# Kernel tuning notes

Hardware: AMD Instinct MI355X
Metric: run time of the kernel (lower is better)

Reference implementation:

```python
import jax, jax.numpy as jnp
import numpy as np

N_IN, D_IN, N_OUT, D_OUT = 1152, 8, 10, 16
ROUTINGS, NUM_BG = 3, 1
C, H, W = 1, 28, 28
BATCH = 128
DEC_IN = N_OUT * D_OUT  # 160, projection_type=None -> dec_feature_size = outcaps_size


def squash(x, axis=-1):
    norm = jnp.linalg.norm(x, axis=axis, keepdims=True)
    scale = norm ** 2 / (1.0 + norm ** 2) / (norm + 1e-8)
    return scale * x


def scale_coef(x, num_bg):
    # x: [B, n_out] or [B, n_out, n_in]; min/max normalize over dim 1,
    # excluding the last num_bg (background) capsules, then floor at 0.5.
    if num_bg > 0:
        xm = x[:, : x.shape[1] - num_bg]
    else:
        xm = x
    mn = jnp.min(xm, axis=1, keepdims=True)
    mx = jnp.max(xm, axis=1, keepdims=True)
    out = (xm - mn) / jnp.maximum(mx - mn, 1e-6)  # vrange (0,1)
    if num_bg > 0:
        out = jnp.concatenate([out, jnp.zeros_like(out[:, :num_bg])], axis=1)
    return jnp.maximum(out, 0.5)


def decode(capsflat, W1, b1, W2, b2, W3, b3):
    # fcn decoder (eval mode: dropout is identity): 160 -> 512 -> 1024 -> C*H*W
    h = jax.nn.relu(capsflat @ W1 + b1)
    h = jax.nn.relu(h @ W2 + b2)
    return jax.nn.sigmoid(h @ W3 + b3)


def setup_inputs() -> dict:
    key = jax.random.key(0)
    ks = jax.random.split(key, 9)
    return {
        'incaps': jax.random.normal(ks[0], (BATCH, N_IN, D_IN), jnp.float32),
        'x_input': jax.random.uniform(ks[1], (BATCH, C, H, W), jnp.float32),
        'weight': 0.1 * jax.random.normal(ks[2], (N_OUT, N_IN, D_OUT, D_IN), jnp.float32),
        'W1': 0.05 * jax.random.normal(ks[3], (DEC_IN, 512), jnp.float32),
        'b1': jnp.zeros((512,), jnp.float32),
        'W2': 0.05 * jax.random.normal(ks[4], (512, 1024), jnp.float32),
        'b2': jnp.zeros((1024,), jnp.float32),
        'W3': 0.05 * jax.random.normal(ks[5], (1024, C * H * W), jnp.float32),
        'b3': jnp.zeros((C * H * W,), jnp.float32),
    }


def reference(incaps, x_input, weight, W1, b1, W2, b2, W3, b3):
    B = incaps.shape[0]
    # outcaps_hat: matmul(weight, incaps[:,None,:,:,None]).squeeze(-1)
    hat = jnp.einsum('nkoi,bki->bnko', weight, incaps)  # [B, n_out, n_in, d_out]
    hat_d = jax.lax.stop_gradient(hat)
    rc = jnp.ones((B, N_OUT, N_IN), hat.dtype)
    eye = jnp.eye(N_OUT, dtype=hat.dtype)
    x_flat = x_input.reshape(B, 1, -1)
    for _ in range(ROUTINGS - 1):
        # squash over capsule dim, weighted sum over input capsules
        outcaps = squash(jnp.sum(rc[..., None] * hat_d, axis=2, keepdims=True))  # [B,n,1,d]
        b = jnp.sum(outcaps * hat_d, axis=-1)  # agreement [B, n_out, n_in]
        c = scale_coef(b, NUM_BG)
        objcaps = outcaps[:, :, 0, :]  # [B, n_out, d_out]
        # get_every_obj_rscore vectorized: mask one object capsule at a time
        masked = objcaps[:, None, :, :] * eye[None, :, :, None]  # [B, n_obj, n_out, d]
        recon = decode(masked.reshape(B, N_OUT, DEC_IN), W1, b1, W2, b2, W3, b3)  # [B,n_obj,CHW]
        rscore = -jnp.sum((x_flat - recon) ** 2, axis=-1)  # neg MSE-sum, [B, n_obj]
        r = scale_coef(rscore, NUM_BG)
        rc = c * r[:, :, None]
    # final iteration uses non-detached hat
    outcaps = squash(jnp.sum(rc[..., None] * hat, axis=2, keepdims=True))
    return outcaps[:, :, 0, :]  # [B, n_out, d_out]
```

## Files before the change

### kernel.cpp

```cpp
#include <hip/hip_runtime.h>
#include <math.h>

#define BATCH  128
#define NIN    1152
#define DIN    8
#define NOUTC  10
#define DOUT   16
#define H1DIM  512
#define H2DIM  1024
#define PIX    784
#define NROWS  (BATCH * NOUTC)
#define MROWS  (BATCH * 9)
#define NBY3   13

typedef __attribute__((ext_vector_type(8))) __bf16 bf16x8;
typedef __attribute__((ext_vector_type(4))) float  f32x4;
typedef __attribute__((ext_vector_type(4))) unsigned int u32x4;

__device__ __forceinline__ float bf2f(unsigned int u) {
    union { unsigned int i; float f; } v; v.i = u << 16; return v.f;
}
__device__ __forceinline__ ushort f2bf(float f) {
    union { float f; unsigned int i; } v; v.f = f;
    unsigned int r = v.i + 0x7FFFu + ((v.i >> 16) & 1u);
    return (ushort)(r >> 16);
}
__device__ __forceinline__ float ldin(const void* p, size_t i, int isbf) {
    return isbf ? bf2f(((const ushort*)p)[i]) : ((const float*)p)[i];
}
__device__ __forceinline__ bf16x8 frag_of(uint4 u) {
    return __builtin_bit_cast(bf16x8, u);
}
__device__ __forceinline__ bf16x8 ld_frag(const ushort* p) {
    return frag_of(*(const uint4*)p);
}
__device__ __forceinline__ float dot8(uint4 a, uint4 b) {
    float s;
    s  = bf2f(a.x & 0xffffu) * bf2f(b.x & 0xffffu);
    s += bf2f(a.x >> 16)     * bf2f(b.x >> 16);
    s += bf2f(a.y & 0xffffu) * bf2f(b.y & 0xffffu);
    s += bf2f(a.y >> 16)     * bf2f(b.y >> 16);
    s += bf2f(a.z & 0xffffu) * bf2f(b.z & 0xffffu);
    s += bf2f(a.z >> 16)     * bf2f(b.z >> 16);
    s += bf2f(a.w & 0xffffu) * bf2f(b.w & 0xffffu);
    s += bf2f(a.w >> 16)     * bf2f(b.w >> 16);
    return s;
}
__device__ __forceinline__ uint4 pack8(float4 a, float4 b) {
    uint4 r;
    r.x = f2bf(a.x) | ((unsigned)f2bf(a.y) << 16);
    r.y = f2bf(a.z) | ((unsigned)f2bf(a.w) << 16);
    r.z = f2bf(b.x) | ((unsigned)f2bf(b.y) << 16);
    r.w = f2bf(b.z) | ((unsigned)f2bf(b.w) << 16);
    return r;
}
__device__ __forceinline__ int detect_bf(const void* w, int* cntS) {
    int tid = threadIdx.x, nt = blockDim.x;
    if (tid == 0) *cntS = 0;
    __syncthreads();
    const ushort* u = (const ushort*)w;
    int c = 0;
    for (int s = tid; s < 512; s += nt) {
        int e = (u[s * 2] >> 7) & 0xFF;
        if (e >= 88 && e <= 140) c++;
    }
    atomicAdd(cntS, c);
    __syncthreads();
    return (*cntS >= 384) ? 1 : 0;
}

struct PrepArgs {
    const void* w;
    const void* src[7];
    ushort*     dst[7];
    int         n[7];
    int*        flag;
};

__global__ __launch_bounds__(256) void prep_kernel(PrepArgs a)
{
    __shared__ int cntS;
    __shared__ ushort tile[32][33];
    int tid = threadIdx.x;
    int isbf = detect_bf(a.w, &cntS);
    int seg = blockIdx.y;
    if (seg == 0 && blockIdx.x == 0 && tid == 0) *a.flag = isbf;

    if (seg <= 4) {
        int n = a.n[seg];
        int stride = gridDim.x * 256;
        ushort* d = a.dst[seg];
        if (isbf) {
            const ushort* s = (const ushort*)a.src[seg];
            for (int i = blockIdx.x * 256 + tid; i < n; i += stride) d[i] = s[i];
        } else {
            const float* s = (const float*)a.src[seg];
            for (int i = blockIdx.x * 256 + tid; i < n; i += stride) d[i] = f2bf(s[i]);
        }
        return;
    }
    int R = (seg == 5) ? H1DIM : H2DIM;
    int C = (seg == 5) ? H2DIM : PIX;
    int tilesX = (seg == 5) ? 32 : 25;
    int tilesY = (seg == 5) ? 16 : 32;
    int t = blockIdx.x;
    if (t >= tilesX * tilesY) return;
    int tx2 = t % tilesX, ty2 = t / tilesX;
    int c0 = tx2 * 32, r0 = ty2 * 32;
    const void* in = a.src[seg];
    ushort* out = a.dst[seg];
    int tx = tid & 31, ty = tid >> 5;
    for (int i = ty; i < 32; i += 8) {
        int r = r0 + i, c = c0 + tx;
        tile[i][tx] = (r < R && c < C) ? f2bf(ldin(in, (size_t)r * C + c, isbf)) : (ushort)0;
    }
    __syncthreads();
    for (int i = ty; i < 32; i += 8) {
        int c = c0 + i, r = r0 + tx;
        if (c < C && r < R) out[(size_t)c * R + r] = tile[tx][i];
    }
}

__global__ __launch_bounds__(256) void hat_build(
    const void* __restrict__ inc,
    const void* __restrict__ w,
    ushort* __restrict__ hatG,
    const int* __restrict__ flagp)
{
    int isbf = *flagp;
    int kc = blockIdx.x, bc = blockIdx.y, n = blockIdx.z;
    int t  = threadIdx.x;
    int k  = kc * 128 + (t >> 1);
    int oh = (t & 1) << 3;

    size_t wbase = ((size_t)n * NIN + k) * DOUT + oh;
    uint4 wr[8];
    if (isbf) {
        const uint4* wp = (const uint4*)((const ushort*)w + wbase * DIN);
        #pragma unroll
        for (int j = 0; j < 8; j++) wr[j] = wp[j];
    } else {
        const float4* wp = (const float4*)((const float*)w + wbase * DIN);
        #pragma unroll
        for (int j = 0; j < 8; j++) wr[j] = pack8(wp[2 * j], wp[2 * j + 1]);
    }

    int b0 = bc * 16;
    #pragma unroll 4
    for (int bl = 0; bl < 16; bl++) {
        int b = b0 + bl;
        size_t ioff = ((size_t)b * NIN + k) * DIN;
        uint4 iu;
        if (isbf) iu = *(const uint4*)((const ushort*)inc + ioff);
        else {
            const float4* ip = (const float4*)((const float*)inc + ioff);
            iu = pack8(ip[0], ip[1]);
        }
        unsigned int h[8];
        #pragma unroll
        for (int j = 0; j < 8; j++) h[j] = f2bf(dot8(wr[j], iu));
        u32x4 ov = { h[0] | (h[1] << 16), h[2] | (h[3] << 16),
                     h[4] | (h[5] << 16), h[6] | (h[7] << 16) };
        __builtin_nontemporal_store(ov,
            (u32x4*)(hatG + (((size_t)(b * NOUTC + n) * NIN + k) * DOUT + oh)));
    }
}

template<bool COMPUTE>
__global__ __launch_bounds__(512, 4) void reduce_pass(
    const ushort* __restrict__ hatG,
    const void*   __restrict__ incRaw,
    const void*   __restrict__ wRaw,
    const ushort* __restrict__ cbuf,
    const float*  __restrict__ partials,
    int iter0,
    const ushort* __restrict__ W1c,
    const ushort* __restrict__ b1c,
    ushort* __restrict__ h1out,
    ushort* __restrict__ bsOut,
    void*   __restrict__ outFinal,
    const int* __restrict__ flagp)
{
    int bn  = blockIdx.x;
    int n   = bn % NOUTC;
    int b   = bn / NOUTC;
    int tid = threadIdx.x;

    __shared__ ushort wSb[NIN];
    __shared__ float  redS[8][16];
    __shared__ float  sumS[16];
    __shared__ float  ocS[16];
    __shared__ float  scaleS;

    int h = tid & 1, kb = tid >> 1;
    int wave = tid >> 6, lane = tid & 63;

    uint4 v[4];
    const ushort* tailS;

    if constexpr (!COMPUTE) {
        __shared__ uint4 hatTail4[256];
        const ushort* hbase = hatG + (size_t)bn * NIN * DOUT;
        #pragma unroll
        for (int j = 0; j < 4; j++)
            v[j] = *(const uint4*)(hbase + ((kb + 256 * j) * DOUT + h * 8));
        if (tid < 256)
            hatTail4[tid] = *(const uint4*)(hbase + 1024 * DOUT + tid * 8);
        tailS = (const ushort*)hatTail4;
    } else {
        __shared__ int cntS;
        __shared__ uint4 hatS4[NIN * DOUT / 8];
        int isbf = detect_bf(wRaw, &cntS);
        size_t wnb = (size_t)n * NIN * DOUT * DIN;
        for (int idx = tid; idx < NIN * DOUT; idx += 512) {
            int k = idx >> 4;
            float s = 0.f;
            #pragma unroll
            for (int i = 0; i < 8; i++)
                s += ldin(wRaw, wnb + (size_t)idx * 8 + i, isbf) *
                     ldin(incRaw, ((size_t)b * NIN + k) * DIN + i, isbf);
            ((ushort*)hatS4)[idx] = f2bf(s);
        }
        __syncthreads();
        const ushort* hbase = (const ushort*)hatS4;
        #pragma unroll
        for (int j = 0; j < 4; j++)
            v[j] = *(const uint4*)(hbase + ((kb + 256 * j) * DOUT + h * 8));
        tailS = hbase + 1024 * DOUT;
    }

    if (!iter0) {
        if (tid < 9) {
            float s = 0.f;
            #pragma unroll
            for (int j = 0; j < NBY3; j++)
                s += partials[(size_t)(b * 9 + tid) * 16 + j];
            sumS[tid] = -s;
        }
        __syncthreads();
        float mn = 1e30f, mx = -1e30f;
        #pragma unroll
        for (int n2 = 0; n2 < 9; n2++) {
            float vv = sumS[n2];
            mn = fminf(mn, vv); mx = fmaxf(mx, vv);
        }
        float den = fmaxf(mx - mn, 1e-6f);
        float rv = (n < 9) ? fmaxf((sumS[n] - mn) / den, 0.5f) : 0.5f;
        const ushort* crow = cbuf + (size_t)bn * NIN;
        for (int k = tid; k < NIN; k += 512)
            wSb[k] = f2bf(bf2f(crow[k]) * rv);
    }
    __syncthreads();

    float acc[8];
    #pragma unroll
    for (int o = 0; o < 8; o++) acc[o] = 0.f;
    #pragma unroll
    for (int j = 0; j < 4; j++) {
        int k = kb + 256 * j;
        float w = iter0 ? 1.f : bf2f(wSb[k]);
        bf16x8 hv = frag_of(v[j]);
        #pragma unroll
        for (int o = 0; o < 8; o++) acc[o] += w * (float)hv[o];
    }
    if (tid < 256) {
        int k = 1024 + kb;
        float w = iter0 ? 1.f : bf2f(wSb[k]);
        bf16x8 hv = ld_frag(tailS + kb * DOUT + h * 8);
        #pragma unroll
        for (int o = 0; o < 8; o++) acc[o] += w * (float)hv[o];
    }
    #pragma unroll
    for (int off = 32; off >= 2; off >>= 1) {
        #pragma unroll
        for (int o = 0; o < 8; o++) acc[o] += __shfl_xor(acc[o], off);
    }
    if (lane < 2) {
        #pragma unroll
        for (int o = 0; o < 8; o++) redS[wave][lane * 8 + o] = acc[o];
    }
    __syncthreads();
    if (tid < 16) {
        float s = 0.f;
        #pragma unroll
        for (int wv = 0; wv < 8; wv++) s += redS[wv][tid];
        sumS[tid] = s;
    }
    __syncthreads();
    if (tid == 0) {
        float n2 = 0.f;
        #pragma unroll
        for (int o = 0; o < 16; o++) n2 += sumS[o] * sumS[o];
        float nrm = sqrtf(n2);
        scaleS = n2 / (1.f + n2) / (nrm + 1e-8f);
    }
    __syncthreads();
    if (tid < 16) {
        float oc = scaleS * sumS[tid];
        ocS[tid] = oc;
        if (outFinal) {
            if (*flagp) ((ushort*)outFinal)[(size_t)bn * 16 + tid] = f2bf(oc);
            else        ((float*) outFinal)[(size_t)bn * 16 + tid] = oc;
        }
    }
    __syncthreads();

    if (bsOut && n < 9) {
        float o0 = ocS[h * 8 + 0], o1 = ocS[h * 8 + 1], o2 = ocS[h * 8 + 2],
              o3 = ocS[h * 8 + 3], o4 = ocS[h * 8 + 4], o5 = ocS[h * 8 + 5],
              o6 = ocS[h * 8 + 6], o7 = ocS[h * 8 + 7];
        #pragma unroll
        for (int j = 0; j < 4; j++) {
            bf16x8 hv = frag_of(v[j]);
            float s = o0 * (float)hv[0] + o1 * (float)hv[1] + o2 * (float)hv[2] +
                      o3 * (float)hv[3] + o4 * (float)hv[4] + o5 * (float)hv[5] +
                      o6 * (float)hv[6] + o7 * (float)hv[7];
            s += __shfl_xor(s, 1);
            if (h == 0) bsOut[(size_t)bn * NIN + kb + 256 * j] = f2bf(s);
        }
        if (tid < 256) {
            bf16x8 hv = ld_frag(tailS + kb * DOUT + h * 8);
            float s = o0 * (float)hv[0] + o1 * (float)hv[1] + o2 * (float)hv[2] +
                      o3 * (float)hv[3] + o4 * (float)hv[4] + o5 * (float)hv[5] +
                      o6 * (float)hv[6] + o7 * (float)hv[7];
            s += __shfl_xor(s, 1);
            if (h == 0) bsOut[(size_t)bn * NIN + 1024 + kb] = f2bf(s);
        }
    }

    if (h1out && n < 9) {
        int col = tid;
        float acc1 = bf2f(b1c[col]);
        #pragma unroll
        for (int i = 0; i < 16; i++)
            acc1 += ocS[i] * bf2f(W1c[(size_t)(n * 16 + i) * H1DIM + col]);
        h1out[(size_t)(b * 9 + n) * H1DIM + col] = f2bf(fmaxf(acc1, 0.f));
    }
}

__global__ __launch_bounds__(256) void gemm2_kernel(
    const ushort* __restrict__ A, const ushort* __restrict__ Bt,
    const ushort* __restrict__ bias, ushort* __restrict__ Cout,
    const ushort* __restrict__ bs, ushort* __restrict__ cbuf)
{
    if (blockIdx.y >= 16) {
        int ci = (blockIdx.y - 16) * 18 + blockIdx.x;
        int base = ci * 4096 + threadIdx.x;
        #pragma unroll 4
        for (int j = 0; j < 16; j++) {
            int pi = base + j * 256;
            int b = pi / NIN, k = pi - b * NIN;
            const ushort* bp = bs + (size_t)b * NOUTC * NIN + k;
            float vv[9], mn = 1e30f, mx = -1e30f;
            #pragma unroll
            for (int n2 = 0; n2 < 9; n2++) {
                vv[n2] = bf2f(bp[n2 * NIN]);
                mn = fminf(mn, vv[n2]); mx = fmaxf(mx, vv[n2]);
            }
            float den = fmaxf(mx - mn, 1e-6f);
            ushort* cp = cbuf + (size_t)b * NOUTC * NIN + k;
            #pragma unroll
            for (int n2 = 0; n2 < 9; n2++)
                cp[n2 * NIN] = f2bf(fmaxf((vv[n2] - mn) / den, 0.5f));
            cp[9 * NIN] = f2bf(0.5f);
        }
        return;
    }
    int m0 = blockIdx.x * 64, n0 = blockIdx.y * 64;
    int tid = threadIdx.x;
    int wave = tid >> 6, lane = tid & 63, quad = lane >> 4, l16 = lane & 15;

    __shared__ uint4 As4[320];
    __shared__ uint4 Bs4[320];
    ushort* As = (ushort*)As4;
    ushort* Bs = (ushort*)Bs4;

    f32x4 acc[4];
    #pragma unroll
    for (int nt = 0; nt < 4; nt++)
        #pragma unroll
        for (int rg = 0; rg < 4; rg++) acc[nt][rg] = 0.f;

    int sMi = tid >> 2, sKk = (tid & 3) * 8;
    int sLds = sMi * 5 + (tid & 3);
    const ushort* Ap = A + (size_t)(m0 + sMi) * H1DIM + sKk;
    const ushort* Bp = Bt + (size_t)(n0 + sMi) * H1DIM + sKk;

    uint4 aR = *(const uint4*)Ap;
    uint4 bR = *(const uint4*)Bp;

    for (int k0 = 0; k0 < H1DIM; k0 += 32) {
        As4[sLds] = aR;
        Bs4[sLds] = bR;
        __syncthreads();
        if (k0 + 32 < H1DIM) {
            aR = *(const uint4*)(Ap + k0 + 32);
            bR = *(const uint4*)(Bp + k0 + 32);
        }
        bf16x8 a = ld_frag(As + (wave * 16 + l16) * 40 + quad * 8);
        #pragma unroll
        for (int nt = 0; nt < 4; nt++) {
            bf16x8 bb = ld_frag(Bs + (nt * 16 + l16) * 40 + quad * 8);
            acc[nt] = __builtin_amdgcn_mfma_f32_16x16x32_bf16(a, bb, acc[nt], 0, 0, 0);
        }
        __syncthreads();
    }

    int rowBase = m0 + wave * 16 + quad * 4;
    #pragma unroll
    for (int nt = 0; nt < 4; nt++) {
        int col = n0 + nt * 16 + l16;
        float bv = bf2f(bias[col]);
        #pragma unroll
        for (int rg = 0; rg < 4; rg++) {
            float v = acc[nt][rg] + bv;
            Cout[(size_t)(rowBase + rg) * H2DIM + col] = f2bf(fmaxf(v, 0.f));
        }
    }
}

__global__ __launch_bounds__(256) void gemm3_kernel(
    const ushort* __restrict__ A, const ushort* __restrict__ Bt,
    const ushort* __restrict__ bias,
    const ushort* __restrict__ xin, float* __restrict__ partials)
{
    int m0 = blockIdx.x * 64, n0 = blockIdx.y * 64;
    int tid = threadIdx.x;
    int wave = tid >> 6, lane = tid & 63, quad = lane >> 4, l16 = lane & 15;

    __shared__ uint4 As4[320];
    __shared__ uint4 Bs4[320];
    ushort* As = (ushort*)As4;
    ushort* Bs = (ushort*)Bs4;

    f32x4 acc[4];
    #pragma unroll
    for (int nt = 0; nt < 4; nt++)
        #pragma unroll
        for (int rg = 0; rg < 4; rg++) acc[nt][rg] = 0.f;

    int sMi = tid >> 2, sKk = (tid & 3) * 8;
    int sLds = sMi * 5 + (tid & 3);
    const ushort* Ap = A + (size_t)(m0 + sMi) * H2DIM + sKk;
    const ushort* Bp = Bt + (size_t)(n0 + sMi) * H2DIM + sKk;
    bool bOK = (n0 + sMi) < PIX;

    uint4 aR = *(const uint4*)Ap;
    uint4 bR = bOK ? *(const uint4*)Bp : make_uint4(0, 0, 0, 0);

    for (int k0 = 0; k0 < H2DIM; k0 += 32) {
        As4[sLds] = aR;
        Bs4[sLds] = bR;
        __syncthreads();
        if (k0 + 32 < H2DIM) {
            aR = *(const uint4*)(Ap + k0 + 32);
            bR = bOK ? *(const uint4*)(Bp + k0 + 32) : make_uint4(0, 0, 0, 0);
        }
        bf16x8 a = ld_frag(As + (wave * 16 + l16) * 40 + quad * 8);
        #pragma unroll
        for (int nt = 0; nt < 4; nt++) {
            bf16x8 bb = ld_frag(Bs + (nt * 16 + l16) * 40 + quad * 8);
            acc[nt] = __builtin_amdgcn_mfma_f32_16x16x32_bf16(a, bb, acc[nt], 0, 0, 0);
        }
        __syncthreads();
    }

    int rowBase = m0 + wave * 16 + quad * 4;
    float vr[4] = {0.f, 0.f, 0.f, 0.f};
    #pragma unroll
    for (int nt = 0; nt < 4; nt++) {
        int col = n0 + nt * 16 + l16;
        if (col < PIX) {
            float bv = bf2f(bias[col]);
            #pragma unroll
            for (int rg = 0; rg < 4; rg++) {
                int row = rowBase + rg;
                int bb = row / 9;
                float z = acc[nt][rg] + bv;
                float s = 1.f / (1.f + __expf(-z));
                float d = bf2f(xin[(size_t)bb * PIX + col]) - s;
                vr[rg] += d * d;
            }
        }
    }
    #pragma unroll
    for (int rg = 0; rg < 4; rg++) {
        float v = vr[rg];
        #pragma unroll
        for (int off = 8; off >= 1; off >>= 1) v += __shfl_xor(v, off, 16);
        if (l16 == 0)
            partials[(size_t)(rowBase + rg) * 16 + blockIdx.y] = v;
    }
}

extern "C" void kernel_launch(void* const* d_in, const int* in_sizes, int n_in,
                              void* d_out, int out_size, void* d_ws, size_t ws_size,
                              hipStream_t stream)
{
    const void* inc = d_in[0];
    const void* x   = d_in[1];
    const void* w   = d_in[2];
    const void* W1  = d_in[3];
    const void* b1  = d_in[4];
    const void* W2  = d_in[5];
    const void* b2  = d_in[6];
    const void* W3  = d_in[7];
    const void* b3  = d_in[8];

    char* p = (char*)d_ws;
    auto alloc = [&](size_t bytes) { void* r = p; p += (bytes + 255) & ~(size_t)255; return r; };
    int*    flagWS    = (int*)alloc(256);
    ushort* bs        = (ushort*)alloc((size_t)NROWS * NIN * 2);
    ushort* cbuf      = (ushort*)alloc((size_t)NROWS * NIN * 2);
    float*  partials  = (float*)alloc((size_t)MROWS * 16 * 4);
    ushort* h1WS      = (ushort*)alloc((size_t)MROWS * H1DIM * 2);
    ushort* h2WS      = (ushort*)alloc((size_t)MROWS * H2DIM * 2);
    ushort* W2T       = (ushort*)alloc((size_t)H2DIM * H1DIM * 2);
    ushort* W3T       = (ushort*)alloc((size_t)PIX * H2DIM * 2);
    ushort* W1c       = (ushort*)alloc((size_t)160 * H1DIM * 2);
    ushort* b1c       = (ushort*)alloc((size_t)H1DIM * 2);
    ushort* b2c       = (ushort*)alloc((size_t)H2DIM * 2);
    ushort* b3c       = (ushort*)alloc((size_t)PIX * 2);
    ushort* xc        = (ushort*)alloc((size_t)BATCH * PIX * 2);
    ushort* hatG      = (ushort*)alloc((size_t)NROWS * NIN * DOUT * 2);
    bool haveHat = ((char*)hatG + (size_t)NROWS * NIN * DOUT * 2) <= ((char*)d_ws + ws_size);

    PrepArgs pa;
    pa.w = w;
    pa.src[0] = W1;  pa.dst[0] = W1c;  pa.n[0] = 160 * H1DIM;
    pa.src[1] = b1;  pa.dst[1] = b1c;  pa.n[1] = H1DIM;
    pa.src[2] = b2;  pa.dst[2] = b2c;  pa.n[2] = H2DIM;
    pa.src[3] = b3;  pa.dst[3] = b3c;  pa.n[3] = PIX;
    pa.src[4] = x;   pa.dst[4] = xc;   pa.n[4] = BATCH * PIX;
    pa.src[5] = W2;  pa.dst[5] = W2T;  pa.n[5] = 0;
    pa.src[6] = W3;  pa.dst[6] = W3T;  pa.n[6] = 0;
    pa.flag = flagWS;
    prep_kernel<<<dim3(800, 7), 256, 0, stream>>>(pa);

    if (haveHat) hat_build<<<dim3(9, 8, NOUTC), 256, 0, stream>>>(inc, w, hatG, flagWS);

    if (haveHat)
        reduce_pass<false><<<NROWS, 512, 0, stream>>>(
            hatG, inc, w, nullptr, nullptr, 1,
            W1c, b1c, h1WS, bs, nullptr, flagWS);
    else
        reduce_pass<true><<<NROWS, 512, 0, stream>>>(
            nullptr, inc, w, nullptr, nullptr, 1,
            W1c, b1c, h1WS, bs, nullptr, flagWS);

    for (int it = 0; it < 2; it++) {
        gemm2_kernel<<<dim3(18, 18), 256, 0, stream>>>(
            h1WS, W2T, b2c, h2WS, bs, cbuf);
        gemm3_kernel<<<dim3(18, NBY3), 256, 0, stream>>>(
            h2WS, W3T, b3c, xc, partials);

        int last = (it == 1);
        ushort* bsO = last ? nullptr : bs;
        ushort* h1o = last ? nullptr : h1WS;
        void*   fin = last ? d_out : nullptr;
        if (haveHat)
            reduce_pass<false><<<NROWS, 512, 0, stream>>>(
                hatG, inc, w, cbuf, partials, 0,
                W1c, b1c, h1o, bsO, fin, flagWS);
        else
            reduce_pass<true><<<NROWS, 512, 0, stream>>>(
                nullptr, inc, w, cbuf, partials, 0,
                W1c, b1c, h1o, bsO, fin, flagWS);
    }
}
```

Before: 215.6 us.

## Retile routing reduce to 384 threads and halve GEMM M-tiles for more blocks

The reduce kernel now uses 384 threads, each owning one full 16-wide input-capsule row over three iterations. This removes the shared-memory tail staging, the two-lane split and one shuffle level. The decoder GEMM2 and GEMM3 kernels switch from 64x64 to 32x64 tiles arranged as 2x2 waves, doubling the grid for better CU occupancy. The partial-sum layout widens to 32 columns, and the c-coefficient side work in GEMM2 is redistributed across the larger grid. The price is reloading more B tiles per output and using more registers per thread in the reduce.

```diff
diff --git a/kernel.cpp b/kernel.cpp
--- a/kernel.cpp
+++ b/kernel.cpp
@@ -11,7 +11,8 @@
 #define PIX    784
 #define NROWS  (BATCH * NOUTC)
 #define MROWS  (BATCH * 9)
-#define NBY3   13
+#define PARTW  32
+#define NPART  26
 
 typedef __attribute__((ext_vector_type(8))) __bf16 bf16x8;
 typedef __attribute__((ext_vector_type(4))) float  f32x4;
@@ -167,7 +168,7 @@
 }
 
 template<bool COMPUTE>
-__global__ __launch_bounds__(512, 4) void reduce_pass(
+__global__ __launch_bounds__(384, 8) void reduce_pass(
     const ushort* __restrict__ hatG,
     const void*   __restrict__ incRaw,
     const void*   __restrict__ wRaw,
@@ -185,56 +186,54 @@
     int n   = bn % NOUTC;
     int b   = bn / NOUTC;
     int tid = threadIdx.x;
+    int wave = tid >> 6, lane = tid & 63;
 
     __shared__ ushort wSb[NIN];
-    __shared__ float  redS[8][16];
+    __shared__ float  redS[6][16];
     __shared__ float  sumS[16];
     __shared__ float  ocS[16];
     __shared__ float  scaleS;
 
-    int h = tid & 1, kb = tid >> 1;
-    int wave = tid >> 6, lane = tid & 63;
-
-    uint4 v[4];
-    const ushort* tailS;
+    uint4 v[3][2];
 
     if constexpr (!COMPUTE) {
-        __shared__ uint4 hatTail4[256];
         const ushort* hbase = hatG + (size_t)bn * NIN * DOUT;
         #pragma unroll
-        for (int j = 0; j < 4; j++)
-            v[j] = *(const uint4*)(hbase + ((kb + 256 * j) * DOUT + h * 8));
-        if (tid < 256)
-            hatTail4[tid] = *(const uint4*)(hbase + 1024 * DOUT + tid * 8);
-        tailS = (const ushort*)hatTail4;
+        for (int j = 0; j < 3; j++) {
+            int k = tid + 384 * j;
+            v[j][0] = *(const uint4*)(hbase + k * DOUT);
+            v[j][1] = *(const uint4*)(hbase + k * DOUT + 8);
+        }
     } else {
         __shared__ int cntS;
         __shared__ uint4 hatS4[NIN * DOUT / 8];
-        int isbf = detect_bf(wRaw, &cntS);
+        int isbf2 = detect_bf(wRaw, &cntS);
         size_t wnb = (size_t)n * NIN * DOUT * DIN;
-        for (int idx = tid; idx < NIN * DOUT; idx += 512) {
+        for (int idx = tid; idx < NIN * DOUT; idx += 384) {
             int k = idx >> 4;
             float s = 0.f;
             #pragma unroll
             for (int i = 0; i < 8; i++)
-                s += ldin(wRaw, wnb + (size_t)idx * 8 + i, isbf) *
-                     ldin(incRaw, ((size_t)b * NIN + k) * DIN + i, isbf);
+                s += ldin(wRaw, wnb + (size_t)idx * 8 + i, isbf2) *
+                     ldin(incRaw, ((size_t)b * NIN + k) * DIN + i, isbf2);
             ((ushort*)hatS4)[idx] = f2bf(s);
         }
         __syncthreads();
         const ushort* hbase = (const ushort*)hatS4;
         #pragma unroll
-        for (int j = 0; j < 4; j++)
-            v[j] = *(const uint4*)(hbase + ((kb + 256 * j) * DOUT + h * 8));
-        tailS = hbase + 1024 * DOUT;
+        for (int j = 0; j < 3; j++) {
+            int k = tid + 384 * j;
+            v[j][0] = *(const uint4*)(hbase + k * DOUT);
+            v[j][1] = *(const uint4*)(hbase + k * DOUT + 8);
+        }
     }
 
     if (!iter0) {
         if (tid < 9) {
             float s = 0.f;
             #pragma unroll
-            for (int j = 0; j < NBY3; j++)
-                s += partials[(size_t)(b * 9 + tid) * 16 + j];
+            for (int j = 0; j < NPART; j++)
+                s += partials[(size_t)(b * 9 + tid) * PARTW + j];
             sumS[tid] = -s;
         }
         __syncthreads();
@@ -247,43 +246,43 @@
         float den = fmaxf(mx - mn, 1e-6f);
         float rv = (n < 9) ? fmaxf((sumS[n] - mn) / den, 0.5f) : 0.5f;
         const ushort* crow = cbuf + (size_t)bn * NIN;
-        for (int k = tid; k < NIN; k += 512)
+        #pragma unroll
+        for (int j = 0; j < 3; j++) {
+            int k = tid + 384 * j;
             wSb[k] = f2bf(bf2f(crow[k]) * rv);
-    }
-    __syncthreads();
-
-    float acc[8];
-    #pragma unroll
-    for (int o = 0; o < 8; o++) acc[o] = 0.f;
-    #pragma unroll
-    for (int j = 0; j < 4; j++) {
-        int k = kb + 256 * j;
+        }
+    }
+    __syncthreads();
+
+    float acc[16];
+    #pragma unroll
+    for (int o = 0; o < 16; o++) acc[o] = 0.f;
+    #pragma unroll
+    for (int j = 0; j < 3; j++) {
+        int k = tid + 384 * j;
         float w = iter0 ? 1.f : bf2f(wSb[k]);
-        bf16x8 hv = frag_of(v[j]);
-        #pragma unroll
-        for (int o = 0; o < 8; o++) acc[o] += w * (float)hv[o];
-    }
-    if (tid < 256) {
-        int k = 1024 + kb;
-        float w = iter0 ? 1.f : bf2f(wSb[k]);
-        bf16x8 hv = ld_frag(tailS + kb * DOUT + h * 8);
-        #pragma unroll
-        for (int o = 0; o < 8; o++) acc[o] += w * (float)hv[o];
-    }
-    #pragma unroll
-    for (int off = 32; off >= 2; off >>= 1) {
-        #pragma unroll
-        for (int o = 0; o < 8; o++) acc[o] += __shfl_xor(acc[o], off);
-    }
-    if (lane < 2) {
-        #pragma unroll
-        for (int o = 0; o < 8; o++) redS[wave][lane * 8 + o] = acc[o];
+        bf16x8 h0 = frag_of(v[j][0]);
+        bf16x8 h1 = frag_of(v[j][1]);
+        #pragma unroll
+        for (int o = 0; o < 8; o++) {
+            acc[o]     += w * (float)h0[o];
+            acc[8 + o] += w * (float)h1[o];
+        }
+    }
+    #pragma unroll
+    for (int off = 32; off >= 1; off >>= 1) {
+        #pragma unroll
+        for (int o = 0; o < 16; o++) acc[o] += __shfl_xor(acc[o], off);
+    }
+    if (lane == 0) {
+        #pragma unroll
+        for (int o = 0; o < 16; o++) redS[wave][o] = acc[o];
     }
     __syncthreads();
     if (tid < 16) {
         float s = 0.f;
         #pragma unroll
-        for (int wv = 0; wv < 8; wv++) s += redS[wv][tid];
+        for (int wv = 0; wv < 6; wv++) s += redS[wv][tid];
         sumS[tid] = s;
     }
     __syncthreads();
@@ -306,35 +305,33 @@
     __syncthreads();
 
     if (bsOut && n < 9) {
-        float o0 = ocS[h * 8 + 0], o1 = ocS[h * 8 + 1], o2 = ocS[h * 8 + 2],
-              o3 = ocS[h * 8 + 3], o4 = ocS[h * 8 + 4], o5 = ocS[h * 8 + 5],
-              o6 = ocS[h * 8 + 6], o7 = ocS[h * 8 + 7];
-        #pragma unroll
-        for (int j = 0; j < 4; j++) {
-            bf16x8 hv = frag_of(v[j]);
-            float s = o0 * (float)hv[0] + o1 * (float)hv[1] + o2 * (float)hv[2] +
-                      o3 * (float)hv[3] + o4 * (float)hv[4] + o5 * (float)hv[5] +
-                      o6 * (float)hv[6] + o7 * (float)hv[7];
-            s += __shfl_xor(s, 1);
-            if (h == 0) bsOut[(size_t)bn * NIN + kb + 256 * j] = f2bf(s);
-        }
-        if (tid < 256) {
-            bf16x8 hv = ld_frag(tailS + kb * DOUT + h * 8);
-            float s = o0 * (float)hv[0] + o1 * (float)hv[1] + o2 * (float)hv[2] +
-                      o3 * (float)hv[3] + o4 * (float)hv[4] + o5 * (float)hv[5] +
-                      o6 * (float)hv[6] + o7 * (float)hv[7];
-            s += __shfl_xor(s, 1);
-            if (h == 0) bsOut[(size_t)bn * NIN + 1024 + kb] = f2bf(s);
+        #pragma unroll
+        for (int j = 0; j < 3; j++) {
+            int k = tid + 384 * j;
+            bf16x8 h0 = frag_of(v[j][0]);
+            bf16x8 h1 = frag_of(v[j][1]);
+            float s = 0.f;
+            #pragma unroll
+            for (int o = 0; o < 8; o++) {
+                s += ocS[o]     * (float)h0[o];
+                s += ocS[8 + o] * (float)h1[o];
+            }
+            bsOut[(size_t)bn * NIN + k] = f2bf(s);
         }
     }
 
     if (h1out && n < 9) {
-        int col = tid;
-        float acc1 = bf2f(b1c[col]);
-        #pragma unroll
-        for (int i = 0; i < 16; i++)
-            acc1 += ocS[i] * bf2f(W1c[(size_t)(n * 16 + i) * H1DIM + col]);
-        h1out[(size_t)(b * 9 + n) * H1DIM + col] = f2bf(fmaxf(acc1, 0.f));
+        #pragma unroll
+        for (int c0 = 0; c0 < 2; c0++) {
+            int col = tid + c0 * 384;
+            if (col < H1DIM) {
+                float acc1 = bf2f(b1c[col]);
+                #pragma unroll
+                for (int i = 0; i < 16; i++)
+                    acc1 += ocS[i] * bf2f(W1c[(size_t)(n * 16 + i) * H1DIM + col]);
+                h1out[(size_t)(b * 9 + n) * H1DIM + col] = f2bf(fmaxf(acc1, 0.f));
+            }
+        }
     }
 }
 
@@ -343,11 +340,12 @@
     const ushort* __restrict__ bias, ushort* __restrict__ Cout,
     const ushort* __restrict__ bs, ushort* __restrict__ cbuf)
 {
+    int tid = threadIdx.x;
     if (blockIdx.y >= 16) {
-        int ci = (blockIdx.y - 16) * 18 + blockIdx.x;
-        int base = ci * 4096 + threadIdx.x;
+        int ci = (blockIdx.y - 16) * 36 + blockIdx.x;
+        int base = ci * 2048 + tid;
         #pragma unroll 4
-        for (int j = 0; j < 16; j++) {
+        for (int j = 0; j < 8; j++) {
             int pi = base + j * 256;
             int b = pi / NIN, k = pi - b * NIN;
             const ushort* bp = bs + (size_t)b * NOUTC * NIN + k;
@@ -366,50 +364,51 @@
         }
         return;
     }
-    int m0 = blockIdx.x * 64, n0 = blockIdx.y * 64;
-    int tid = threadIdx.x;
+    int m0 = blockIdx.x * 32, n0 = blockIdx.y * 64;
     int wave = tid >> 6, lane = tid & 63, quad = lane >> 4, l16 = lane & 15;
 
-    __shared__ uint4 As4[320];
+    __shared__ uint4 As4[160];
     __shared__ uint4 Bs4[320];
     ushort* As = (ushort*)As4;
     ushort* Bs = (ushort*)Bs4;
 
-    f32x4 acc[4];
-    #pragma unroll
-    for (int nt = 0; nt < 4; nt++)
+    f32x4 acc[2];
+    #pragma unroll
+    for (int nt = 0; nt < 2; nt++)
         #pragma unroll
         for (int rg = 0; rg < 4; rg++) acc[nt][rg] = 0.f;
 
     int sMi = tid >> 2, sKk = (tid & 3) * 8;
-    int sLds = sMi * 5 + (tid & 3);
-    const ushort* Ap = A + (size_t)(m0 + sMi) * H1DIM + sKk;
+    int sLdsA = (sMi & 31) * 5 + (tid & 3);
+    int sLdsB = sMi * 5 + (tid & 3);
+    const ushort* Ap = A + (size_t)(m0 + (sMi & 31)) * H1DIM + sKk;
     const ushort* Bp = Bt + (size_t)(n0 + sMi) * H1DIM + sKk;
 
-    uint4 aR = *(const uint4*)Ap;
+    uint4 aR = (tid < 128) ? *(const uint4*)Ap : make_uint4(0, 0, 0, 0);
     uint4 bR = *(const uint4*)Bp;
 
+    int r0 = (wave & 1) * 16, c0 = (wave >> 1) * 32;
     for (int k0 = 0; k0 < H1DIM; k0 += 32) {
-        As4[sLds] = aR;
-        Bs4[sLds] = bR;
+        if (tid < 128) As4[sLdsA] = aR;
+        Bs4[sLdsB] = bR;
         __syncthreads();
         if (k0 + 32 < H1DIM) {
-            aR = *(const uint4*)(Ap + k0 + 32);
+            if (tid < 128) aR = *(const uint4*)(Ap + k0 + 32);
             bR = *(const uint4*)(Bp + k0 + 32);
         }
-        bf16x8 a = ld_frag(As + (wave * 16 + l16) * 40 + quad * 8);
-        #pragma unroll
-        for (int nt = 0; nt < 4; nt++) {
-            bf16x8 bb = ld_frag(Bs + (nt * 16 + l16) * 40 + quad * 8);
+        bf16x8 a = ld_frag(As + (r0 + l16) * 40 + quad * 8);
+        #pragma unroll
+        for (int nt = 0; nt < 2; nt++) {
+            bf16x8 bb = ld_frag(Bs + (c0 + nt * 16 + l16) * 40 + quad * 8);
             acc[nt] = __builtin_amdgcn_mfma_f32_16x16x32_bf16(a, bb, acc[nt], 0, 0, 0);
         }
         __syncthreads();
     }
 
-    int rowBase = m0 + wave * 16 + quad * 4;
-    #pragma unroll
-    for (int nt = 0; nt < 4; nt++) {
-        int col = n0 + nt * 16 + l16;
+    int rowBase = m0 + (wave & 1) * 16 + quad * 4;
+    #pragma unroll
+    for (int nt = 0; nt < 2; nt++) {
+        int col = n0 + (wave >> 1) * 32 + nt * 16 + l16;
         float bv = bf2f(bias[col]);
         #pragma unroll
         for (int rg = 0; rg < 4; rg++) {
@@ -424,52 +423,54 @@
     const ushort* __restrict__ bias,
     const ushort* __restrict__ xin, float* __restrict__ partials)
 {
-    int m0 = blockIdx.x * 64, n0 = blockIdx.y * 64;
     int tid = threadIdx.x;
+    int m0 = blockIdx.x * 32, n0 = blockIdx.y * 64;
     int wave = tid >> 6, lane = tid & 63, quad = lane >> 4, l16 = lane & 15;
 
-    __shared__ uint4 As4[320];
+    __shared__ uint4 As4[160];
     __shared__ uint4 Bs4[320];
     ushort* As = (ushort*)As4;
     ushort* Bs = (ushort*)Bs4;
 
-    f32x4 acc[4];
-    #pragma unroll
-    for (int nt = 0; nt < 4; nt++)
+    f32x4 acc[2];
+    #pragma unroll
+    for (int nt = 0; nt < 2; nt++)
         #pragma unroll
         for (int rg = 0; rg < 4; rg++) acc[nt][rg] = 0.f;
 
     int sMi = tid >> 2, sKk = (tid & 3) * 8;
-    int sLds = sMi * 5 + (tid & 3);
-    const ushort* Ap = A + (size_t)(m0 + sMi) * H2DIM + sKk;
+    int sLdsA = (sMi & 31) * 5 + (tid & 3);
+    int sLdsB = sMi * 5 + (tid & 3);
+    const ushort* Ap = A + (size_t)(m0 + (sMi & 31)) * H2DIM + sKk;
     const ushort* Bp = Bt + (size_t)(n0 + sMi) * H2DIM + sKk;
     bool bOK = (n0 + sMi) < PIX;
 
-    uint4 aR = *(const uint4*)Ap;
+    uint4 aR = (tid < 128) ? *(const uint4*)Ap : make_uint4(0, 0, 0, 0);
     uint4 bR = bOK ? *(const uint4*)Bp : make_uint4(0, 0, 0, 0);
 
+    int r0 = (wave & 1) * 16, c0 = (wave >> 1) * 32;
     for (int k0 = 0; k0 < H2DIM; k0 += 32) {
-        As4[sLds] = aR;
-        Bs4[sLds] = bR;
+        if (tid < 128) As4[sLdsA] = aR;
+        Bs4[sLdsB] = bR;
         __syncthreads();
         if (k0 + 32 < H2DIM) {
-            aR = *(const uint4*)(Ap + k0 + 32);
-            bR = bOK ? *(const uint4*)(Bp + k0 + 32) : make_uint4(0, 0, 0, 0);
-        }
-        bf16x8 a = ld_frag(As + (wave * 16 + l16) * 40 + quad * 8);
-        #pragma unroll
-        for (int nt = 0; nt < 4; nt++) {
-            bf16x8 bb = ld_frag(Bs + (nt * 16 + l16) * 40 + quad * 8);
+            if (tid < 128) aR = *(const uint4*)(Ap + k0 + 32);
+            if (bOK) bR = *(const uint4*)(Bp + k0 + 32);
+        }
+        bf16x8 a = ld_frag(As + (r0 + l16) * 40 + quad * 8);
+        #pragma unroll
+        for (int nt = 0; nt < 2; nt++) {
+            bf16x8 bb = ld_frag(Bs + (c0 + nt * 16 + l16) * 40 + quad * 8);
             acc[nt] = __builtin_amdgcn_mfma_f32_16x16x32_bf16(a, bb, acc[nt], 0, 0, 0);
         }
         __syncthreads();
     }
 
-    int rowBase = m0 + wave * 16 + quad * 4;
+    int rowBase = m0 + (wave & 1) * 16 + quad * 4;
     float vr[4] = {0.f, 0.f, 0.f, 0.f};
     #pragma unroll
-    for (int nt = 0; nt < 4; nt++) {
-        int col = n0 + nt * 16 + l16;
+    for (int nt = 0; nt < 2; nt++) {
+        int col = n0 + (wave >> 1) * 32 + nt * 16 + l16;
         if (col < PIX) {
             float bv = bf2f(bias[col]);
             #pragma unroll
@@ -489,7 +490,7 @@
         #pragma unroll
         for (int off = 8; off >= 1; off >>= 1) v += __shfl_xor(v, off, 16);
         if (l16 == 0)
-            partials[(size_t)(rowBase + rg) * 16 + blockIdx.y] = v;
+            partials[(size_t)(rowBase + rg) * PARTW + blockIdx.y * 2 + (wave >> 1)] = v;
     }
 }
 
@@ -512,7 +513,7 @@
     int*    flagWS    = (int*)alloc(256);
     ushort* bs        = (ushort*)alloc((size_t)NROWS * NIN * 2);
     ushort* cbuf      = (ushort*)alloc((size_t)NROWS * NIN * 2);
-    float*  partials  = (float*)alloc((size_t)MROWS * 16 * 4);
+    float*  partials  = (float*)alloc((size_t)MROWS * PARTW * 4);
     ushort* h1WS      = (ushort*)alloc((size_t)MROWS * H1DIM * 2);
     ushort* h2WS      = (ushort*)alloc((size_t)MROWS * H2DIM * 2);
     ushort* W2T       = (ushort*)alloc((size_t)H2DIM * H1DIM * 2);
@@ -540,18 +541,18 @@
     if (haveHat) hat_build<<<dim3(9, 8, NOUTC), 256, 0, stream>>>(inc, w, hatG, flagWS);
 
     if (haveHat)
-        reduce_pass<false><<<NROWS, 512, 0, stream>>>(
+        reduce_pass<false><<<NROWS, 384, 0, stream>>>(
             hatG, inc, w, nullptr, nullptr, 1,
             W1c, b1c, h1WS, bs, nullptr, flagWS);
     else
-        reduce_pass<true><<<NROWS, 512, 0, stream>>>(
+        reduce_pass<true><<<NROWS, 384, 0, stream>>>(
             nullptr, inc, w, nullptr, nullptr, 1,
             W1c, b1c, h1WS, bs, nullptr, flagWS);
 
     for (int it = 0; it < 2; it++) {
-        gemm2_kernel<<<dim3(18, 18), 256, 0, stream>>>(
+        gemm2_kernel<<<dim3(36, 18), 256, 0, stream>>>(
             h1WS, W2T, b2c, h2WS, bs, cbuf);
-        gemm3_kernel<<<dim3(18, NBY3), 256, 0, stream>>>(
+        gemm3_kernel<<<dim3(36, 13), 256, 0, stream>>>(
             h2WS, W3T, b3c, xc, partials);
 
         int last = (it == 1);
@@ -559,11 +560,11 @@
         ushort* h1o = last ? nullptr : h1WS;
         void*   fin = last ? d_out : nullptr;
         if (haveHat)
-            reduce_pass<false><<<NROWS, 512, 0, stream>>>(
+            reduce_pass<false><<<NROWS, 384, 0, stream>>>(
                 hatG, inc, w, cbuf, partials, 0,
                 W1c, b1c, h1o, bsO, fin, flagWS);
         else
-            reduce_pass<true><<<NROWS, 512, 0, stream>>>(
+            reduce_pass<true><<<NROWS, 384, 0, stream>>>(
                 nullptr, inc, w, cbuf, partials, 0,
                 W1c, b1c, h1o, bsO, fin, flagWS);
     }
```

Result: slower. 236.1 us (+9.5%).
